# Optimization experiments

Hardware: AMD Instinct MI355X
Metric: run time of the kernel (lower is better)

Reference implementation:

```python
import jax, jax.numpy as jnp
import numpy as np

N, L, H, Q = 64, 258, 1024, 256
WINDOW = 16.0
DEV_POW = 128.0  # 2 * (window/2)^2, Luong local-p sigma = D/2


def setup_inputs() -> dict:
    key = jax.random.key(0)
    k1, k2, k3, k4, k5, k6 = jax.random.split(key, 6)
    encoder_outputs = jax.random.normal(k1, (N, L, H), dtype=jnp.float32)
    decoder_h_t = jax.random.normal(k2, (N, Q, H), dtype=jnp.float32)
    src_len = jax.random.randint(k3, (N,), 32, L + 1).astype(jnp.int32)
    # window centers within each source sentence
    p_t = jax.random.uniform(k4, (N,), dtype=jnp.float32) * (src_len.astype(jnp.float32) - 1.0)
    W_a = jax.random.normal(k5, (H, H), dtype=jnp.float32) * (1.0 / np.sqrt(H))
    W_c = jax.random.normal(k6, (H, 2 * H), dtype=jnp.float32) * (1.0 / np.sqrt(2 * H))
    return {"encoder_outputs": encoder_outputs, "decoder_h_t": decoder_h_t,
            "src_len": src_len, "p_t": p_t, "W_a": W_a, "W_c": W_c}


def reference(encoder_outputs, decoder_h_t, src_len, p_t, W_a, W_c):
    n, l, h = encoder_outputs.shape
    idx = jnp.arange(l, dtype=jnp.float32)  # index_matrix, length == max_length == L

    # local_p window: [p_t - D, p_t + D], clamped to [0, src_len]
    src_end = src_len.astype(jnp.float32)
    attn_start = jnp.maximum(p_t - WINDOW, 0.0)          # [N]
    attn_end = jnp.minimum(p_t + WINDOW, src_end)        # [N]
    mask = (idx[None, :] < attn_start[:, None]) | (idx[None, :] > attn_end[:, None])  # [N,L]

    # Luong 'general' score: h_t^T W_a h_s -> [N,Q,L]
    score = jnp.einsum('nqh,hk,nlk->nql', decoder_h_t, W_a, encoder_outputs)

    score = jnp.where(mask[:, None, :], -1e9, score)
    align = jax.nn.softmax(score, axis=2)                 # [N,Q,L]

    # gaussian reweighting centered at p_t
    gauss = jnp.exp(-((idx[None, :] - p_t[:, None]) ** 2) / DEV_POW)  # [N,L]
    align = align * gauss[:, None, :]

    context = jnp.einsum('nql,nlh->nqh', align, encoder_outputs)      # [N,Q,H]
    cat = jnp.concatenate([context, decoder_h_t], axis=2)             # [N,Q,2H]
    return jnp.tanh(cat @ W_c.T)                                      # [N,Q,H]
```

## Files before the change

kernel.cpp:

```cpp
#include <hip/hip_runtime.h>
#include <hip/hip_bf16.h>
#include <cstdint>

#define DEVINL __device__ __forceinline__

typedef __attribute__((ext_vector_type(8))) short short8;
typedef __attribute__((ext_vector_type(4))) float f32x4;
typedef __attribute__((ext_vector_type(4))) unsigned short u16x4;

static constexpr int NB = 64, LL = 258, HH = 1024, QQ = 256;
static constexpr int WROWS = 33;
static constexpr int MU = 2176;
static constexpr int VTN = 4096;

static constexpr size_t OFF_META = 0;
static constexpr size_t SZ_WE   = (size_t)MU * HH * 2;
static constexpr size_t OFF_WEHI = 1024;
static constexpr size_t OFF_WELO = OFF_WEHI + SZ_WE;
static constexpr size_t OFF_WAHI = OFF_WELO + SZ_WE;
static constexpr size_t OFF_WALO = OFF_WAHI + (size_t)HH * HH * 2;
static constexpr size_t OFF_WCBF = OFF_WALO + (size_t)HH * HH * 2;
static constexpr size_t OFF_HBF  = OFF_WCBF + (size_t)HH * 2 * HH * 2;
static constexpr size_t OFF_U    = OFF_HBF + (size_t)NB * QQ * HH * 2;
static constexpr size_t OFF_UHI  = OFF_U;
static constexpr size_t OFF_ULO  = OFF_U + (size_t)MU * HH * 2;
static constexpr size_t OFF_CTX  = OFF_U + (size_t)MU * HH * 4;
static constexpr size_t OFF_VT   = OFF_CTX + (size_t)NB * QQ * HH * 2;

DEVINL unsigned short f2bf(float x) {
    union { float f; uint32_t u; } v; v.f = x;
    uint32_t u = v.u;
    uint32_t r = (u + 0x7FFFu + ((u >> 16) & 1u)) >> 16;
    return (unsigned short)r;
}
DEVINL float bf2f(unsigned short b) {
    union { uint32_t u; float f; } v; v.u = ((uint32_t)b) << 16;
    return v.f;
}

template <typename T>
DEVINL void lds_load16(const T* g, T* l) {
    __builtin_amdgcn_global_load_lds(
        (const __attribute__((address_space(1))) void*)g,
        (__attribute__((address_space(3))) void*)l, 16, 0, 0);
}

DEVINL float fast_tanh(float x) {
    float e = __expf(2.0f * x);
    return 1.0f - 2.0f / (e + 1.0f);
}

__global__ void k_window(const float* __restrict__ pt, const int* __restrict__ slen,
                         int* __restrict__ meta) {
    int n = threadIdx.x;
    if (n >= NB) return;
    float p = pt[n];
    float se = (float)slen[n];
    float s = fmaxf(p - 16.0f, 0.0f);
    float e = fminf(p + 16.0f, se);
    int ls = (int)ceilf(s);
    int le = (int)floorf(e); if (le > LL - 1) le = LL - 1;
    int lc = le - ls + 1;
    if (lc < 0) lc = 0;
    if (lc > WROWS) lc = WROWS;
    meta[n] = ls; meta[64 + n] = lc;
}

__global__ __launch_bounds__(256) void k_split(const float* __restrict__ x,
                                               unsigned short* __restrict__ hi,
                                               unsigned short* __restrict__ lo, int count4) {
    int i = blockIdx.x * 256 + threadIdx.x;
    if (i >= count4) return;
    f32x4 v = ((const f32x4*)x)[i];
    u16x4 h, l;
#pragma unroll
    for (int j = 0; j < 4; ++j) {
        unsigned short hb = f2bf(v[j]);
        h[j] = hb;
        l[j] = f2bf(v[j] - bf2f(hb));
    }
    ((u16x4*)hi)[i] = h;
    ((u16x4*)lo)[i] = l;
}

__global__ __launch_bounds__(256) void k_tobf(const float* __restrict__ x,
                                              unsigned short* __restrict__ hi, int count4) {
    int i = blockIdx.x * 256 + threadIdx.x;
    if (i >= count4) return;
    f32x4 v = ((const f32x4*)x)[i];
    u16x4 h;
#pragma unroll
    for (int j = 0; j < 4; ++j) h[j] = f2bf(v[j]);
    ((u16x4*)hi)[i] = h;
}

__global__ __launch_bounds__(256) void k_gather(const float* __restrict__ enc,
                                                const int* __restrict__ meta,
                                                unsigned short* __restrict__ whi,
                                                unsigned short* __restrict__ wlo) {
    int r = blockIdx.x;
    int t = threadIdx.x;
    const float* src = nullptr;
    bool valid = false;
    if (r < NB * WROWS) {
        int n = r / WROWS, li = r - n * WROWS;
        int ls = meta[n], lc = meta[64 + n];
        if (li < lc) { valid = true; src = enc + ((size_t)n * LL + ls + li) * HH; }
    }
    f32x4 v;
    if (valid) v = ((const f32x4*)src)[t];
    else { v[0] = 0.f; v[1] = 0.f; v[2] = 0.f; v[3] = 0.f; }
    u16x4 h, l;
#pragma unroll
    for (int j = 0; j < 4; ++j) {
        unsigned short hb = f2bf(v[j]);
        h[j] = hb;
        l[j] = f2bf(v[j] - bf2f(hb));
    }
    size_t o = (size_t)r * HH / 4 + t;
    ((u16x4*)whi)[o] = h;
    ((u16x4*)wlo)[o] = l;
}

__global__ __launch_bounds__(256) void k_ugemm64(const unsigned short* __restrict__ Ahi,
                                                 const unsigned short* __restrict__ Alo,
                                                 const unsigned short* __restrict__ Bhi,
                                                 const unsigned short* __restrict__ Blo,
                                                 unsigned short* __restrict__ Uhi,
                                                 unsigned short* __restrict__ Ulo) {
    __shared__ unsigned short sAh[2][64 * 32], sAl[2][64 * 32], sBh[2][64 * 32], sBl[2][64 * 32];
    const int tid = threadIdx.x;
    const int w = tid >> 6, lane = tid & 63;
    const int m0 = blockIdx.y * 64, n0 = blockIdx.x * 64;
    const int wr = w >> 1, wc = w & 1;
    const int r16 = lane & 15, khalf = lane >> 4;
    const int srow = tid >> 2;
    const int scol = ((tid & 3) ^ ((tid >> 3) & 3)) * 8;
    const int ldso = tid * 8;
    const int kslot = (khalf ^ ((r16 >> 1) & 3)) * 8;
    f32x4 acc[2][2] = {};

    auto stage = [&](int buf, int kb) {
        lds_load16(Ahi + (size_t)(m0 + srow) * HH + kb + scol, &sAh[buf][ldso]);
        lds_load16(Alo + (size_t)(m0 + srow) * HH + kb + scol, &sAl[buf][ldso]);
        lds_load16(Bhi + (size_t)(n0 + srow) * HH + kb + scol, &sBh[buf][ldso]);
        lds_load16(Blo + (size_t)(n0 + srow) * HH + kb + scol, &sBl[buf][ldso]);
    };

    stage(0, 0);
    for (int t = 0; t < 32; ++t) {
        const int buf = t & 1;
        asm volatile("s_waitcnt vmcnt(0)" ::: "memory");
        __builtin_amdgcn_s_barrier();
        short8 ah[2], al[2], bh[2], bl[2];
#pragma unroll
        for (int f = 0; f < 2; ++f) {
            int ai = (wr * 32 + f * 16 + r16) * 32 + kslot;
            ah[f] = *(const short8*)&sAh[buf][ai];
            al[f] = *(const short8*)&sAl[buf][ai];
            int bi = (wc * 32 + f * 16 + r16) * 32 + kslot;
            bh[f] = *(const short8*)&sBh[buf][bi];
            bl[f] = *(const short8*)&sBl[buf][bi];
        }
        if (t + 1 < 32) stage(buf ^ 1, (t + 1) * 32);
        asm volatile("s_waitcnt lgkmcnt(0)" ::: "memory");
        __builtin_amdgcn_sched_barrier(0);
#pragma unroll
        for (int mf = 0; mf < 2; ++mf)
#pragma unroll
            for (int nf = 0; nf < 2; ++nf) {
                acc[mf][nf] = __builtin_amdgcn_mfma_f32_16x16x32_bf16(ah[mf], bh[nf], acc[mf][nf], 0, 0, 0);
                acc[mf][nf] = __builtin_amdgcn_mfma_f32_16x16x32_bf16(ah[mf], bl[nf], acc[mf][nf], 0, 0, 0);
                acc[mf][nf] = __builtin_amdgcn_mfma_f32_16x16x32_bf16(al[mf], bh[nf], acc[mf][nf], 0, 0, 0);
            }
        __builtin_amdgcn_s_barrier();
    }
    const int rg = lane >> 4;
#pragma unroll
    for (int mf = 0; mf < 2; ++mf)
#pragma unroll
        for (int nf = 0; nf < 2; ++nf)
#pragma unroll
            for (int r = 0; r < 4; ++r) {
                int m = m0 + wr * 32 + mf * 16 + rg * 4 + r;
                int nn = n0 + wc * 32 + nf * 16 + r16;
                float v = acc[mf][nf][r];
                unsigned short h = f2bf(v);
                Uhi[(size_t)m * HH + nn] = h;
                Ulo[(size_t)m * HH + nn] = f2bf(v - bf2f(h));
            }
}

__global__ __launch_bounds__(256) void k_vgemm64(const unsigned short* __restrict__ Wc1,
                                                 const unsigned short* __restrict__ Bhi,
                                                 const unsigned short* __restrict__ Blo,
                                                 unsigned short* __restrict__ VT) {
    __shared__ unsigned short sA[2][64 * 32], sBh[2][64 * 32], sBl[2][64 * 32];
    const int tid = threadIdx.x;
    const int w = tid >> 6, lane = tid & 63;
    const int m0 = blockIdx.y * 64, n0 = blockIdx.x * 64;
    const int wr = w >> 1, wc = w & 1;
    const int r16 = lane & 15, khalf = lane >> 4;
    const int srow = tid >> 2;
    const int scol = ((tid & 3) ^ ((tid >> 3) & 3)) * 8;
    const int ldso = tid * 8;
    const int kslot = (khalf ^ ((r16 >> 1) & 3)) * 8;
    f32x4 acc[2][2] = {};

    auto stage = [&](int buf, int kb) {
        lds_load16(Wc1 + (size_t)(m0 + srow) * (2 * HH) + kb + scol, &sA[buf][ldso]);
        lds_load16(Bhi + (size_t)(n0 + srow) * HH + kb + scol, &sBh[buf][ldso]);
        lds_load16(Blo + (size_t)(n0 + srow) * HH + kb + scol, &sBl[buf][ldso]);
    };

    stage(0, 0);
    for (int t = 0; t < 32; ++t) {
        const int buf = t & 1;
        asm volatile("s_waitcnt vmcnt(0)" ::: "memory");
        __builtin_amdgcn_s_barrier();
        short8 af[2], bh[2], bl[2];
#pragma unroll
        for (int f = 0; f < 2; ++f) {
            af[f] = *(const short8*)&sA[buf][(wr * 32 + f * 16 + r16) * 32 + kslot];
            int bi = (wc * 32 + f * 16 + r16) * 32 + kslot;
            bh[f] = *(const short8*)&sBh[buf][bi];
            bl[f] = *(const short8*)&sBl[buf][bi];
        }
        if (t + 1 < 32) stage(buf ^ 1, (t + 1) * 32);
        asm volatile("s_waitcnt lgkmcnt(0)" ::: "memory");
        __builtin_amdgcn_sched_barrier(0);
#pragma unroll
        for (int mf = 0; mf < 2; ++mf)
#pragma unroll
            for (int nf = 0; nf < 2; ++nf) {
                acc[mf][nf] = __builtin_amdgcn_mfma_f32_16x16x32_bf16(af[mf], bh[nf], acc[mf][nf], 0, 0, 0);
                acc[mf][nf] = __builtin_amdgcn_mfma_f32_16x16x32_bf16(af[mf], bl[nf], acc[mf][nf], 0, 0, 0);
            }
        __builtin_amdgcn_s_barrier();
    }
    const int rg = lane >> 4;
#pragma unroll
    for (int mf = 0; mf < 2; ++mf)
#pragma unroll
        for (int nf = 0; nf < 2; ++nf)
#pragma unroll
            for (int r = 0; r < 4; ++r) {
                int o = m0 + wr * 32 + mf * 16 + rg * 4 + r;
                int wrow = n0 + wc * 32 + nf * 16 + r16;
                int n = wrow / WROWS, li = wrow - n * WROWS;
                if (n < NB)
                    VT[(size_t)o * VTN + n * 64 + li] = f2bf(acc[mf][nf][r]);
            }
}

__global__ __launch_bounds__(256) void k_attn2(const float* __restrict__ ht,
                                               const unsigned short* __restrict__ Uhi,
                                               const unsigned short* __restrict__ Ulo,
                                               const unsigned short* __restrict__ VT,
                                               const float* __restrict__ pt,
                                               const int* __restrict__ meta,
                                               unsigned short* __restrict__ ctx) {
    __shared__ float sPart[4][32 * 48];
    __shared__ float sScore[32 * 48];
    __shared__ unsigned short sPhi[32 * 72];
    __shared__ unsigned short sPlo[32 * 72];

    const int tid = threadIdx.x;
    const int w = tid >> 6, lane = tid & 63;
    const int n = blockIdx.x >> 3, q0 = (blockIdx.x & 7) * 32;
    const int ls = meta[n], lc = meta[64 + n];
    const float p = pt[n];
    const int r16 = lane & 15, khalf = lane >> 4, rg = lane >> 4;

    const float* hbase = ht + ((size_t)(n * QQ + q0)) * HH;
    const unsigned short* uhbase = Uhi + (size_t)n * WROWS * HH;
    const unsigned short* ulbase = Ulo + (size_t)n * WROWS * HH;

    f32x4 acc[2][3] = {};
    for (int ks = 0; ks < 8; ++ks) {
        int kcol = w * 256 + ks * 32 + khalf * 8;
        short8 ah[2], al[2];
#pragma unroll
        for (int mf = 0; mf < 2; ++mf) {
            const float* src = hbase + (size_t)(mf * 16 + r16) * HH + kcol;
            f32x4 v0 = *(const f32x4*)src;
            f32x4 v1 = *(const f32x4*)(src + 4);
            float vv[8] = {v0[0], v0[1], v0[2], v0[3], v1[0], v1[1], v1[2], v1[3]};
#pragma unroll
            for (int j = 0; j < 8; ++j) {
                unsigned short hb = f2bf(vv[j]);
                ah[mf][j] = (short)hb;
                al[mf][j] = (short)f2bf(vv[j] - bf2f(hb));
            }
        }
#pragma unroll
        for (int nf = 0; nf < 3; ++nf) {
            size_t uoff = (size_t)(nf * 16 + r16) * HH + kcol;
            short8 bh = *(const short8*)(uhbase + uoff);
            short8 bl = *(const short8*)(ulbase + uoff);
#pragma unroll
            for (int mf = 0; mf < 2; ++mf) {
                acc[mf][nf] = __builtin_amdgcn_mfma_f32_16x16x32_bf16(ah[mf], bh, acc[mf][nf], 0, 0, 0);
                acc[mf][nf] = __builtin_amdgcn_mfma_f32_16x16x32_bf16(ah[mf], bl, acc[mf][nf], 0, 0, 0);
                acc[mf][nf] = __builtin_amdgcn_mfma_f32_16x16x32_bf16(al[mf], bh, acc[mf][nf], 0, 0, 0);
            }
        }
    }
#pragma unroll
    for (int mf = 0; mf < 2; ++mf)
#pragma unroll
        for (int nf = 0; nf < 3; ++nf)
#pragma unroll
            for (int r = 0; r < 4; ++r)
                sPart[w][(mf * 16 + rg * 4 + r) * 48 + nf * 16 + r16] = acc[mf][nf][r];
    __syncthreads();

    {
        int q = tid >> 3, g = tid & 7;
        float sc6[6];
#pragma unroll
        for (int s = 0; s < 6; ++s) {
            int li = g + 8 * s;
            int o = q * 48 + li;
            sc6[s] = sPart[0][o] + sPart[1][o] + sPart[2][o] + sPart[3][o];
        }
        float mx = -1e30f;
#pragma unroll
        for (int s = 0; s < 6; ++s) { int li = g + 8 * s; if (li < lc) mx = fmaxf(mx, sc6[s]); }
        for (int off = 1; off < 8; off <<= 1) mx = fmaxf(mx, __shfl_xor(mx, off, 8));
        float sum = 0.f, ex[6];
#pragma unroll
        for (int s = 0; s < 6; ++s) {
            int li = g + 8 * s;
            float e = (li < lc) ? __expf(sc6[s] - mx) : 0.f;
            ex[s] = e; sum += e;
        }
        for (int off = 1; off < 8; off <<= 1) sum += __shfl_xor(sum, off, 8);
        float inv = 1.0f / sum;
#pragma unroll
        for (int s = 0; s < 6; ++s) {
            int li = g + 8 * s;
            float d = (float)(ls + li) - p;
            float gs = __expf(-(d * d) * (1.0f / 128.0f));
            sScore[q * 48 + li] = ex[s] * inv * gs;
        }
    }
    __syncthreads();

    {
        int row = tid >> 3, c0 = (tid & 7) * 8;
#pragma unroll
        for (int j = 0; j < 8; ++j) {
            int c = c0 + j;
            float pv = (c < 48) ? sScore[row * 48 + c] : 0.f;
            unsigned short hb = f2bf(pv);
            sPhi[row * 72 + c] = hb;
            sPlo[row * 72 + c] = f2bf(pv - bf2f(hb));
        }
    }
    __syncthreads();

    short8 pa[2][2], plq[2][2];
#pragma unroll
    for (int mf = 0; mf < 2; ++mf)
#pragma unroll
        for (int ks = 0; ks < 2; ++ks) {
            pa[mf][ks]  = *(const short8*)&sPhi[(mf * 16 + r16) * 72 + ks * 32 + khalf * 8];
            plq[mf][ks] = *(const short8*)&sPlo[(mf * 16 + r16) * 72 + ks * 32 + khalf * 8];
        }
    const unsigned short* vtb = VT + n * 64 + khalf * 8;
#pragma unroll
    for (int half = 0; half < 2; ++half) {
        f32x4 accB[2][8] = {};
        const int hcol0 = w * 256 + half * 128;
#pragma unroll
        for (int nf = 0; nf < 8; ++nf) {
            const int o = hcol0 + nf * 16 + r16;
#pragma unroll
            for (int ks = 0; ks < 2; ++ks) {
                short8 bfrag = *(const short8*)(vtb + (size_t)o * VTN + ks * 32);
#pragma unroll
                for (int mf = 0; mf < 2; ++mf) {
                    accB[mf][nf] = __builtin_amdgcn_mfma_f32_16x16x32_bf16(pa[mf][ks], bfrag, accB[mf][nf], 0, 0, 0);
                    accB[mf][nf] = __builtin_amdgcn_mfma_f32_16x16x32_bf16(plq[mf][ks], bfrag, accB[mf][nf], 0, 0, 0);
                }
            }
        }
#pragma unroll
        for (int mf = 0; mf < 2; ++mf)
#pragma unroll
            for (int nf = 0; nf < 8; ++nf)
#pragma unroll
                for (int r = 0; r < 4; ++r)
                    ctx[(size_t)(n * QQ + q0 + mf * 16 + rg * 4 + r) * HH + hcol0 + nf * 16 + r16] =
                        f2bf(accB[mf][nf][r]);
    }
}

#define RD_A(dst, buf, mh, mq, ksub) \
    dst = *(const short8*)&sA[(buf) * 16384 + (mh) * 8192 + \
        (wr * 64 + (mq) * 16 + r16) * 64 + ((((ksub) * 4 + kg) ^ (r16 & 7)) * 8)];
#define RD_B(dst, buf, nh, nq, ksub) \
    dst = *(const short8*)&sB[(buf) * 16384 + (nh) * 8192 + \
        (wc * 32 + (nq) * 16 + r16) * 64 + ((((ksub) * 4 + kg) ^ (r16 & 7)) * 8)];
#define MFMA_QUAD(MH, NH) \
    _Pragma("unroll") \
    for (int mq = 0; mq < 4; ++mq) { \
        _Pragma("unroll") \
        for (int nq = 0; nq < 2; ++nq) { \
            f32x4 c = acc[(MH) * 4 + mq][(NH) * 2 + nq]; \
            c = __builtin_amdgcn_mfma_f32_16x16x32_bf16(a[mq][0], b[nq][0], c, 0, 0, 0); \
            c = __builtin_amdgcn_mfma_f32_16x16x32_bf16(a[mq][1], b[nq][1], c, 0, 0, 0); \
            acc[(MH) * 4 + mq][(NH) * 2 + nq] = c; \
        } \
    }
#define PHASE_SYNC() \
    __builtin_amdgcn_s_barrier(); \
    asm volatile("s_waitcnt lgkmcnt(0)" ::: "memory"); \
    __builtin_amdgcn_sched_barrier(0);

__global__ __launch_bounds__(512, 1) void k_out_gemm256(
    const unsigned short* __restrict__ Ahf,
    const unsigned short* __restrict__ Bt,
    const unsigned short* __restrict__ Cadd,
    float* __restrict__ out) {
    extern __shared__ unsigned short lds[];
    unsigned short* sA = lds;
    unsigned short* sB = lds + 32768;

    const int tid = threadIdx.x;
    const int wid = tid >> 6, lane = tid & 63;
    const int bid = blockIdx.x;
    const int swz = (bid & 7) * 32 + (bid >> 3);
    const int mt = swz >> 2, ntile = swz & 3;
    const int m0 = mt * 256, n0 = ntile * 256;
    const int wr = wid >> 2, wc = wid & 3;
    const int r16 = lane & 15, kg = lane >> 4;

    const int srow = lane >> 3;
    const int kswz = ((lane & 7) ^ srow) * 8;

    f32x4 acc[8][4] = {};

    auto stage_tile = [&](int buf, int kb) {
#pragma unroll
        for (int half = 0; half < 2; ++half) {
#pragma unroll
            for (int i = 0; i < 2; ++i) {
                int r = half * 128 + i * 64 + wid * 8 + srow;
                lds_load16(Ahf + (size_t)(m0 + r) * HH + kb + kswz,
                           sA + buf * 16384 + half * 8192 + i * 4096 + wid * 512);
            }
#pragma unroll
            for (int i = 0; i < 2; ++i) {
                int r = half * 128 + i * 64 + wid * 8 + srow;
                lds_load16(Bt + (size_t)(n0 + r) * (2 * HH) + 1024 + kb + kswz,
                           sB + buf * 16384 + half * 8192 + i * 4096 + wid * 512);
            }
        }
    };

    stage_tile(0, 0);
    asm volatile("s_waitcnt vmcnt(4)" ::: "memory");
    __builtin_amdgcn_s_barrier();

    short8 a[4][2], b[2][2];
    for (int t = 0; t < 16; ++t) {
        const int buf = t & 1;
#pragma unroll
        for (int mq = 0; mq < 4; ++mq) { RD_A(a[mq][0], buf, 0, mq, 0) RD_A(a[mq][1], buf, 0, mq, 1) }
#pragma unroll
        for (int nq = 0; nq < 2; ++nq) { RD_B(b[nq][0], buf, 0, nq, 0) RD_B(b[nq][1], buf, 0, nq, 1) }
        if (t + 1 < 16) stage_tile(buf ^ 1, (t + 1) * 64);
        PHASE_SYNC()
        __builtin_amdgcn_s_setprio(1);
        MFMA_QUAD(0, 0)
        __builtin_amdgcn_s_setprio(0);
        if (t + 1 < 16) { asm volatile("s_waitcnt vmcnt(8)" ::: "memory"); }
        else            { asm volatile("s_waitcnt vmcnt(0)" ::: "memory"); }
        __builtin_amdgcn_s_barrier();
#pragma unroll
        for (int nq = 0; nq < 2; ++nq) { RD_B(b[nq][0], buf, 1, nq, 0) RD_B(b[nq][1], buf, 1, nq, 1) }
        PHASE_SYNC()
        __builtin_amdgcn_s_setprio(1);
        MFMA_QUAD(0, 1)
        __builtin_amdgcn_s_setprio(0);
        __builtin_amdgcn_s_barrier();
#pragma unroll
        for (int mq = 0; mq < 4; ++mq) { RD_A(a[mq][0], buf, 1, mq, 0) RD_A(a[mq][1], buf, 1, mq, 1) }
        PHASE_SYNC()
        __builtin_amdgcn_s_setprio(1);
        MFMA_QUAD(1, 1)
        __builtin_amdgcn_s_setprio(0);
        __builtin_amdgcn_s_barrier();
#pragma unroll
        for (int nq = 0; nq < 2; ++nq) { RD_B(b[nq][0], buf, 0, nq, 0) RD_B(b[nq][1], buf, 0, nq, 1) }
        PHASE_SYNC()
        __builtin_amdgcn_s_setprio(1);
        MFMA_QUAD(1, 0)
        __builtin_amdgcn_s_setprio(0);
        asm volatile("s_waitcnt vmcnt(4)" ::: "memory");
        __builtin_amdgcn_s_barrier();
    }

#pragma unroll
    for (int m = 0; m < 8; ++m)
#pragma unroll
        for (int n = 0; n < 4; ++n) {
            int row = m0 + (m >> 2) * 128 + wr * 64 + (m & 3) * 16 + kg * 4;
            int col = n0 + (n >> 1) * 128 + wc * 32 + (n & 1) * 16 + r16;
#pragma unroll
            for (int r = 0; r < 4; ++r) {
                float cadd = bf2f(Cadd[(size_t)(row + r) * HH + col]);
                out[(size_t)(row + r) * HH + col] = fast_tanh(acc[m][n][r] + cadd);
            }
        }
}

extern "C" void kernel_launch(void* const* d_in, const int* in_sizes, int n_in,
                              void* d_out, int out_size, void* d_ws, size_t ws_size,
                              hipStream_t stream) {
    const float* enc  = (const float*)d_in[0];
    const float* ht   = (const float*)d_in[1];
    const int*   slen = (const int*)d_in[2];
    const float* pt   = (const float*)d_in[3];
    const float* Wa   = (const float*)d_in[4];
    const float* Wc   = (const float*)d_in[5];
    float* out = (float*)d_out;

    char* ws = (char*)d_ws;
    int* meta = (int*)(ws + OFF_META);
    unsigned short* wehi = (unsigned short*)(ws + OFF_WEHI);
    unsigned short* welo = (unsigned short*)(ws + OFF_WELO);
    unsigned short* wahi = (unsigned short*)(ws + OFF_WAHI);
    unsigned short* walo = (unsigned short*)(ws + OFF_WALO);
    unsigned short* wcbf = (unsigned short*)(ws + OFF_WCBF);
    unsigned short* hbf  = (unsigned short*)(ws + OFF_HBF);
    unsigned short* uhi  = (unsigned short*)(ws + OFF_UHI);
    unsigned short* ulo  = (unsigned short*)(ws + OFF_ULO);
    unsigned short* ctx  = (unsigned short*)(ws + OFF_CTX);
    unsigned short* vt   = (unsigned short*)(ws + OFF_VT);

    hipFuncSetAttribute((const void*)k_out_gemm256,
                        hipFuncAttributeMaxDynamicSharedMemorySize, 131072);

    hipLaunchKernelGGL(k_window, dim3(1), dim3(64), 0, stream, pt, slen, meta);
    hipLaunchKernelGGL(k_split, dim3((HH * HH / 4) / 256), dim3(256), 0, stream,
                       Wa, wahi, walo, HH * HH / 4);
    hipLaunchKernelGGL(k_tobf, dim3((HH * 2 * HH / 4) / 256), dim3(256), 0, stream,
                       Wc, wcbf, HH * 2 * HH / 4);
    hipLaunchKernelGGL(k_tobf, dim3((NB * QQ * HH / 4) / 256), dim3(256), 0, stream,
                       ht, hbf, NB * QQ * HH / 4);
    hipLaunchKernelGGL(k_gather, dim3(MU), dim3(256), 0, stream, enc, meta, wehi, welo);
    hipLaunchKernelGGL(k_ugemm64, dim3(HH / 64, MU / 64), dim3(256), 0, stream,
                       wehi, welo, wahi, walo, uhi, ulo);
    hipLaunchKernelGGL(k_vgemm64, dim3(MU / 64, HH / 64), dim3(256), 0, stream,
                       wcbf, wehi, welo, vt);
    hipLaunchKernelGGL(k_attn2, dim3(NB * 8), dim3(256), 0, stream,
                       ht, uhi, ulo, vt, pt, meta, ctx);
    hipLaunchKernelGGL(k_out_gemm256, dim3(256), dim3(512), 131072, stream,
                       hbf, wcbf, ctx, out);
}
```

Before: 170.3 us.

## Fuse prep kernels into one launch and pre-swizzle context for epilogue

Merges the window computation, weight/activation bf16 conversion and encoder gather kernels into a single k_prep launch, and recomputes each batch's window inline instead of reading a meta buffer. This removes four kernel launches and their serialization gaps. The attention kernel now writes the context in a tile-packed layout that matches the output GEMM's thread mapping, so the epilogue loads it with 16-byte vector reads instead of scattered 2-byte reads. The cost is a tight coupling between the two kernels' tile layouts.

After: 158.4 us. 1.08x faster.

```diff
diff --git a/kernel.cpp b/kernel.cpp
--- a/kernel.cpp
+++ b/kernel.cpp
@@ -50,76 +50,80 @@
     return 1.0f - 2.0f / (e + 1.0f);
 }
 
-__global__ void k_window(const float* __restrict__ pt, const int* __restrict__ slen,
-                         int* __restrict__ meta) {
-    int n = threadIdx.x;
-    if (n >= NB) return;
-    float p = pt[n];
-    float se = (float)slen[n];
+DEVINL void window_of(float p, int sl, int& ls, int& lc) {
+    float se = (float)sl;
     float s = fmaxf(p - 16.0f, 0.0f);
     float e = fminf(p + 16.0f, se);
-    int ls = (int)ceilf(s);
+    ls = (int)ceilf(s);
     int le = (int)floorf(e); if (le > LL - 1) le = LL - 1;
-    int lc = le - ls + 1;
+    lc = le - ls + 1;
     if (lc < 0) lc = 0;
     if (lc > WROWS) lc = WROWS;
-    meta[n] = ls; meta[64 + n] = lc;
-}
-
-__global__ __launch_bounds__(256) void k_split(const float* __restrict__ x,
-                                               unsigned short* __restrict__ hi,
-                                               unsigned short* __restrict__ lo, int count4) {
-    int i = blockIdx.x * 256 + threadIdx.x;
-    if (i >= count4) return;
-    f32x4 v = ((const f32x4*)x)[i];
-    u16x4 h, l;
-#pragma unroll
-    for (int j = 0; j < 4; ++j) {
-        unsigned short hb = f2bf(v[j]);
-        h[j] = hb;
-        l[j] = f2bf(v[j] - bf2f(hb));
-    }
-    ((u16x4*)hi)[i] = h;
-    ((u16x4*)lo)[i] = l;
-}
-
-__global__ __launch_bounds__(256) void k_tobf(const float* __restrict__ x,
-                                              unsigned short* __restrict__ hi, int count4) {
-    int i = blockIdx.x * 256 + threadIdx.x;
-    if (i >= count4) return;
-    f32x4 v = ((const f32x4*)x)[i];
-    u16x4 h;
-#pragma unroll
-    for (int j = 0; j < 4; ++j) h[j] = f2bf(v[j]);
-    ((u16x4*)hi)[i] = h;
-}
-
-__global__ __launch_bounds__(256) void k_gather(const float* __restrict__ enc,
-                                                const int* __restrict__ meta,
-                                                unsigned short* __restrict__ whi,
-                                                unsigned short* __restrict__ wlo) {
-    int r = blockIdx.x;
-    int t = threadIdx.x;
-    const float* src = nullptr;
-    bool valid = false;
-    if (r < NB * WROWS) {
-        int n = r / WROWS, li = r - n * WROWS;
-        int ls = meta[n], lc = meta[64 + n];
-        if (li < lc) { valid = true; src = enc + ((size_t)n * LL + ls + li) * HH; }
-    }
-    f32x4 v;
-    if (valid) v = ((const f32x4*)src)[t];
-    else { v[0] = 0.f; v[1] = 0.f; v[2] = 0.f; v[3] = 0.f; }
-    u16x4 h, l;
-#pragma unroll
-    for (int j = 0; j < 4; ++j) {
-        unsigned short hb = f2bf(v[j]);
-        h[j] = hb;
-        l[j] = f2bf(v[j] - bf2f(hb));
-    }
-    size_t o = (size_t)r * HH / 4 + t;
-    ((u16x4*)whi)[o] = h;
-    ((u16x4*)wlo)[o] = l;
+}
+
+__global__ __launch_bounds__(256) void k_prep(const float* __restrict__ enc,
+                                              const float* __restrict__ ht,
+                                              const float* __restrict__ pt,
+                                              const int* __restrict__ slen,
+                                              const float* __restrict__ Wa,
+                                              const float* __restrict__ Wc,
+                                              unsigned short* __restrict__ wehi,
+                                              unsigned short* __restrict__ welo,
+                                              unsigned short* __restrict__ wahi,
+                                              unsigned short* __restrict__ walo,
+                                              unsigned short* __restrict__ wcbf,
+                                              unsigned short* __restrict__ hbf) {
+    const int b = blockIdx.x, t = threadIdx.x;
+    if (b < MU) {
+        int r = b;
+        const float* src = nullptr;
+        bool valid = false;
+        if (r < NB * WROWS) {
+            int n = r / WROWS, li = r - n * WROWS;
+            int ls, lc;
+            window_of(pt[n], slen[n], ls, lc);
+            if (li < lc) { valid = true; src = enc + ((size_t)n * LL + ls + li) * HH; }
+        }
+        f32x4 v;
+        if (valid) v = ((const f32x4*)src)[t];
+        else { v[0] = 0.f; v[1] = 0.f; v[2] = 0.f; v[3] = 0.f; }
+        u16x4 h, l;
+#pragma unroll
+        for (int j = 0; j < 4; ++j) {
+            unsigned short hb = f2bf(v[j]);
+            h[j] = hb;
+            l[j] = f2bf(v[j] - bf2f(hb));
+        }
+        size_t o = (size_t)r * HH / 4 + t;
+        ((u16x4*)wehi)[o] = h;
+        ((u16x4*)welo)[o] = l;
+    } else if (b < MU + 1024) {
+        int i = (b - MU) * 256 + t;
+        f32x4 v = ((const f32x4*)Wa)[i];
+        u16x4 h, l;
+#pragma unroll
+        for (int j = 0; j < 4; ++j) {
+            unsigned short hb = f2bf(v[j]);
+            h[j] = hb;
+            l[j] = f2bf(v[j] - bf2f(hb));
+        }
+        ((u16x4*)wahi)[i] = h;
+        ((u16x4*)walo)[i] = l;
+    } else if (b < MU + 1024 + 2048) {
+        int i = (b - MU - 1024) * 256 + t;
+        f32x4 v = ((const f32x4*)Wc)[i];
+        u16x4 h;
+#pragma unroll
+        for (int j = 0; j < 4; ++j) h[j] = f2bf(v[j]);
+        ((u16x4*)wcbf)[i] = h;
+    } else {
+        int i = (b - MU - 3072) * 256 + t;
+        f32x4 v = ((const f32x4*)ht)[i];
+        u16x4 h;
+#pragma unroll
+        for (int j = 0; j < 4; ++j) h[j] = f2bf(v[j]);
+        ((u16x4*)hbf)[i] = h;
+    }
 }
 
 __global__ __launch_bounds__(256) void k_ugemm64(const unsigned short* __restrict__ Ahi,
@@ -258,8 +262,8 @@
                                                const unsigned short* __restrict__ Ulo,
                                                const unsigned short* __restrict__ VT,
                                                const float* __restrict__ pt,
-                                               const int* __restrict__ meta,
-                                               unsigned short* __restrict__ ctx) {
+                                               const int* __restrict__ slen,
+                                               unsigned short* __restrict__ ctxP) {
     __shared__ float sPart[4][32 * 48];
     __shared__ float sScore[32 * 48];
     __shared__ unsigned short sPhi[32 * 72];
@@ -268,7 +272,8 @@
     const int tid = threadIdx.x;
     const int w = tid >> 6, lane = tid & 63;
     const int n = blockIdx.x >> 3, q0 = (blockIdx.x & 7) * 32;
-    const int ls = meta[n], lc = meta[64 + n];
+    int ls, lc;
+    window_of(pt[n], slen[n], ls, lc);
     const float p = pt[n];
     const int r16 = lane & 15, khalf = lane >> 4, rg = lane >> 4;
 
@@ -369,6 +374,7 @@
             plq[mf][ks] = *(const short8*)&sPlo[(mf * 16 + r16) * 72 + ks * 32 + khalf * 8];
         }
     const unsigned short* vtb = VT + n * 64 + khalf * 8;
+    const size_t tile16 = (size_t)(n * 4 + w) * 16;
 #pragma unroll
     for (int half = 0; half < 2; ++half) {
         f32x4 accB[2][8] = {};
@@ -387,13 +393,24 @@
             }
         }
 #pragma unroll
-        for (int mf = 0; mf < 2; ++mf)
-#pragma unroll
-            for (int nf = 0; nf < 8; ++nf)
-#pragma unroll
-                for (int r = 0; r < 4; ++r)
-                    ctx[(size_t)(n * QQ + q0 + mf * 16 + rg * 4 + r) * HH + hcol0 + nf * 16 + r16] =
-                        f2bf(accB[mf][nf][r]);
+        for (int mf = 0; mf < 2; ++mf) {
+            const int br = q0 + mf * 16;
+            const int m  = (br >> 7) * 4 + ((br >> 4) & 3);
+            const int wr2 = (br >> 6) & 1;
+            const int ib = m * 2 + half;
+#pragma unroll
+            for (int nfp = 0; nfp < 4; ++nfp) {
+                short8 pk;
+#pragma unroll
+                for (int r = 0; r < 4; ++r) {
+                    pk[r]     = (short)f2bf(accB[mf][2 * nfp][r]);
+                    pk[4 + r] = (short)f2bf(accB[mf][2 * nfp + 1][r]);
+                }
+                const int tid_o = wr2 * 256 + nfp * 64 + lane;
+                size_t off = (((tile16 + ib) * 512) + tid_o) * 8;
+                *(short8*)&ctxP[off] = pk;
+            }
+        }
     }
 }
 
@@ -422,7 +439,7 @@
 __global__ __launch_bounds__(512, 1) void k_out_gemm256(
     const unsigned short* __restrict__ Ahf,
     const unsigned short* __restrict__ Bt,
-    const unsigned short* __restrict__ Cadd,
+    const unsigned short* __restrict__ Cp,
     float* __restrict__ out) {
     extern __shared__ unsigned short lds[];
     unsigned short* sA = lds;
@@ -503,15 +520,21 @@
         __builtin_amdgcn_s_barrier();
     }
 
+    const unsigned short* cbase = Cp + (((size_t)(mt * 4 + ntile)) * 16) * 512 * 8;
+    short8 cv[16];
+#pragma unroll
+    for (int ib = 0; ib < 16; ++ib)
+        cv[ib] = *(const short8*)&cbase[((size_t)ib * 512 + tid) * 8];
 #pragma unroll
     for (int m = 0; m < 8; ++m)
 #pragma unroll
         for (int n = 0; n < 4; ++n) {
             int row = m0 + (m >> 2) * 128 + wr * 64 + (m & 3) * 16 + kg * 4;
             int col = n0 + (n >> 1) * 128 + wc * 32 + (n & 1) * 16 + r16;
+            const int ib = m * 2 + (n >> 1);
 #pragma unroll
             for (int r = 0; r < 4; ++r) {
-                float cadd = bf2f(Cadd[(size_t)(row + r) * HH + col]);
+                float cadd = bf2f((unsigned short)cv[ib][(n & 1) * 4 + r]);
                 out[(size_t)(row + r) * HH + col] = fast_tanh(acc[m][n][r] + cadd);
             }
         }
@@ -529,7 +552,6 @@
     float* out = (float*)d_out;
 
     char* ws = (char*)d_ws;
-    int* meta = (int*)(ws + OFF_META);
     unsigned short* wehi = (unsigned short*)(ws + OFF_WEHI);
     unsigned short* welo = (unsigned short*)(ws + OFF_WELO);
     unsigned short* wahi = (unsigned short*)(ws + OFF_WAHI);
@@ -538,26 +560,20 @@
     unsigned short* hbf  = (unsigned short*)(ws + OFF_HBF);
     unsigned short* uhi  = (unsigned short*)(ws + OFF_UHI);
     unsigned short* ulo  = (unsigned short*)(ws + OFF_ULO);
-    unsigned short* ctx  = (unsigned short*)(ws + OFF_CTX);
+    unsigned short* ctxP = (unsigned short*)(ws + OFF_CTX);
     unsigned short* vt   = (unsigned short*)(ws + OFF_VT);
 
     hipFuncSetAttribute((const void*)k_out_gemm256,
                         hipFuncAttributeMaxDynamicSharedMemorySize, 131072);
 
-    hipLaunchKernelGGL(k_window, dim3(1), dim3(64), 0, stream, pt, slen, meta);
-    hipLaunchKernelGGL(k_split, dim3((HH * HH / 4) / 256), dim3(256), 0, stream,
-                       Wa, wahi, walo, HH * HH / 4);
-    hipLaunchKernelGGL(k_tobf, dim3((HH * 2 * HH / 4) / 256), dim3(256), 0, stream,
-                       Wc, wcbf, HH * 2 * HH / 4);
-    hipLaunchKernelGGL(k_tobf, dim3((NB * QQ * HH / 4) / 256), dim3(256), 0, stream,
-                       ht, hbf, NB * QQ * HH / 4);
-    hipLaunchKernelGGL(k_gather, dim3(MU), dim3(256), 0, stream, enc, meta, wehi, welo);
+    hipLaunchKernelGGL(k_prep, dim3(MU + 1024 + 2048 + 16384), dim3(256), 0, stream,
+                       enc, ht, pt, slen, Wa, Wc, wehi, welo, wahi, walo, wcbf, hbf);
     hipLaunchKernelGGL(k_ugemm64, dim3(HH / 64, MU / 64), dim3(256), 0, stream,
                        wehi, welo, wahi, walo, uhi, ulo);
     hipLaunchKernelGGL(k_vgemm64, dim3(MU / 64, HH / 64), dim3(256), 0, stream,
                        wcbf, wehi, welo, vt);
     hipLaunchKernelGGL(k_attn2, dim3(NB * 8), dim3(256), 0, stream,
-                       ht, uhi, ulo, vt, pt, meta, ctx);
+                       ht, uhi, ulo, vt, pt, slen, ctxP);
     hipLaunchKernelGGL(k_out_gemm256, dim3(256), dim3(512), 131072, stream,
-                       hbf, wcbf, ctx, out);
-}
+                       hbf, wcbf, ctxP, out);
+}
```
